# Performance work log

Measured on AMD Instinct MI355X. Metric: run time of the kernel, lower is better.

Reference implementation:

```python
import jax, jax.numpy as jnp
import numpy as np

N, E, IN, OUT, H = 100000, 1600000, 128, 128, 4
C = OUT // H
NEG_SLOPE = 0.2  # PyG GATConv default LeakyReLU slope
BN_EPS = 1e-5


def setup_inputs() -> dict:
    key = jax.random.key(0)
    k = jax.random.split(key, 6)
    x = jax.random.normal(k[0], (N, IN), dtype=jnp.float32)
    edge_index = jax.random.randint(k[1], (2, E), 0, N, dtype=jnp.int64)
    W = jax.random.normal(k[2], (IN, H * C), dtype=jnp.float32) / np.sqrt(IN)
    att_src = jax.random.normal(k[3], (H, C), dtype=jnp.float32) * 0.1
    att_dst = jax.random.normal(k[4], (H, C), dtype=jnp.float32) * 0.1
    gat_bias = jnp.zeros((H * C,), dtype=jnp.float32)
    bn_gamma = jnp.ones((OUT,), dtype=jnp.float32)
    bn_beta = jnp.zeros((OUT,), dtype=jnp.float32)
    return {"x": x, "edge_index": edge_index, "W": W, "att_src": att_src,
            "att_dst": att_dst, "gat_bias": gat_bias, "bn_gamma": bn_gamma,
            "bn_beta": bn_beta}


def reference(x, edge_index, W, att_src, att_dst, gat_bias, bn_gamma, bn_beta):
    n = x.shape[0]
    # GATConv: linear transform, per-head view [N,H,C]
    h = (x @ W).reshape(n, H, C)
    # add self loops (PyG default add_self_loops=True)
    loop = jnp.arange(n, dtype=edge_index.dtype)
    src = jnp.concatenate([edge_index[0], loop])  # message source j
    dst = jnp.concatenate([edge_index[1], loop])  # message target i
    # per-node attention logits [N,H]
    a_src = jnp.einsum('nhc,hc->nh', h, att_src)
    a_dst = jnp.einsum('nhc,hc->nh', h, att_dst)
    # per-edge logits [Etot,H], LeakyReLU, segment softmax over dst
    e = jax.nn.leaky_relu(a_src[src] + a_dst[dst], NEG_SLOPE)
    m = jax.ops.segment_max(e, dst, num_segments=n)
    e = jnp.exp(e - m[dst])
    s = jax.ops.segment_sum(e, dst, num_segments=n)
    alpha = e / (s[dst] + 1e-16)  # dropout(p=0.3) is identity at eval
    # weighted scatter-add aggregation
    msg = h[src] * alpha[:, :, None]  # [Etot,H,C]
    out = jax.ops.segment_sum(msg, dst, num_segments=n).reshape(n, H * C)
    out = out + gat_bias
    # BatchNorm1d (batch statistics, biased var)
    mean = jnp.mean(out, axis=0)
    var = jnp.var(out, axis=0)
    out = bn_gamma * (out - mean) * jax.lax.rsqrt(var + BN_EPS) + bn_beta
    # residual (proj is Identity since in_ch == out_ch) + ReLU
    return jax.nn.relu(out + x)
```

## Files before the change

### kernel.cpp

```cpp
#include <hip/hip_runtime.h>

#define NEG 0.2f
#define EPB 8192
#define NB64MAX 1568
#define CAPB_MAX 1536

typedef short short8 __attribute__((ext_vector_type(8)));
typedef float floatx4 __attribute__((ext_vector_type(4)));

__device__ __forceinline__ float bf_lo(unsigned int u) { return __uint_as_float(u << 16); }
__device__ __forceinline__ float bf_hi(unsigned int u) { return __uint_as_float(u & 0xffff0000u); }
__device__ __forceinline__ unsigned short f2bf(float f) {
    unsigned int u = __float_as_uint(f);
    return (unsigned short)((u + 0x7fff + ((u >> 16) & 1)) >> 16);
}

__global__ __launch_bounds__(256) void k_wconv(const float* __restrict__ W,
                                               unsigned short* __restrict__ Wtb) {
    int i = blockIdx.x * 256 + threadIdx.x;
    int n = i >> 7, k = i & 127;
    Wtb[n * 128 + k] = f2bf(W[k * 128 + n]);
}

__global__ __launch_bounds__(256) void k_gemm(const float* __restrict__ x,
                                              const unsigned short* __restrict__ Wtb,
                                              const float* __restrict__ att_src,
                                              const float* __restrict__ att_dst,
                                              unsigned short* __restrict__ hb,
                                              unsigned int* __restrict__ asd, int N) {
    __shared__ unsigned short As[64 * 128];
    __shared__ unsigned short Bs[128 * 128];
    int t = threadIdx.x;
    int r0 = blockIdx.x * 64;
#pragma unroll
    for (int p = 0; p < 8; p++) {
        int idx = t + 256 * p;
        int row = idx >> 5, c4 = idx & 31;
        float4 v = make_float4(0.f, 0.f, 0.f, 0.f);
        if (r0 + row < N) v = *(const float4*)&x[(size_t)(r0 + row) * 128 + c4 * 4];
        int kb = c4 >> 1;
        unsigned short* d = &As[row * 128 + ((kb ^ (row & 7)) << 3) + (c4 & 1) * 4];
        d[0] = f2bf(v.x); d[1] = f2bf(v.y); d[2] = f2bf(v.z); d[3] = f2bf(v.w);
    }
#pragma unroll
    for (int p = 0; p < 8; p++) {
        int idx = t + 256 * p;
        int n = idx >> 4, k8 = idx & 15;
        *(short8*)&Bs[n * 128 + ((k8 ^ (n & 7)) << 3)] = *(const short8*)&Wtb[n * 128 + k8 * 8];
    }
    __syncthreads();
    int lane = t & 63, wv = t >> 6;
    int m16 = lane & 15, quad = lane >> 4;
    int rowbase = wv * 16;
    floatx4 acc[8];
#pragma unroll
    for (int c = 0; c < 8; c++) acc[c] = (floatx4){0.f, 0.f, 0.f, 0.f};
#pragma unroll
    for (int ks = 0; ks < 4; ks++) {
        int arow = rowbase + m16;
        short8 a = *(const short8*)&As[arow * 128 + (((ks * 4 + quad) ^ (arow & 7)) << 3)];
#pragma unroll
        for (int c = 0; c < 8; c++) {
            int brow = c * 16 + m16;
            short8 b = *(const short8*)&Bs[brow * 128 + (((ks * 4 + quad) ^ (brow & 7)) << 3)];
            acc[c] = __builtin_amdgcn_mfma_f32_16x16x32_bf16(a, b, acc[c], 0, 0, 0);
        }
    }
    float ps[4][4], pd[4][4];
#pragma unroll
    for (int hd = 0; hd < 4; hd++)
#pragma unroll
        for (int r = 0; r < 4; r++) { ps[hd][r] = 0.f; pd[hd][r] = 0.f; }
#pragma unroll
    for (int c = 0; c < 8; c++) {
        int col = c * 16 + m16;
        float as_ = att_src[col], ad_ = att_dst[col];
        int hd = c >> 1;
#pragma unroll
        for (int r = 0; r < 4; r++) {
            float v = acc[c][r];
            int row = r0 + rowbase + quad * 4 + r;
            if (row < N) hb[(size_t)row * 128 + col] = f2bf(v);
            ps[hd][r] = fmaf(v, as_, ps[hd][r]);
            pd[hd][r] = fmaf(v, ad_, pd[hd][r]);
        }
    }
#pragma unroll
    for (int off = 1; off < 16; off <<= 1) {
#pragma unroll
        for (int hd = 0; hd < 4; hd++)
#pragma unroll
            for (int r = 0; r < 4; r++) {
                ps[hd][r] += __shfl_xor(ps[hd][r], off, 16);
                pd[hd][r] += __shfl_xor(pd[hd][r], off, 16);
            }
    }
    if (m16 == 0) {
#pragma unroll
        for (int r = 0; r < 4; r++) {
            int row = r0 + rowbase + quad * 4 + r;
            if (row < N)
#pragma unroll
                for (int hd = 0; hd < 4; hd++)
                    asd[row * 4 + hd] = ((unsigned int)f2bf(pd[hd][r]) << 16) | f2bf(ps[hd][r]);
        }
    }
}

__global__ __launch_bounds__(512) void k_bin3(const int* __restrict__ ei,
                                              int* __restrict__ gcur,
                                              unsigned int* __restrict__ pairs,
                                              int E, int NB, int CAPB) {
    __shared__ int cnt[NB64MAX];
    __shared__ int lbase[NB64MAX];
    int t = threadIdx.x;
    for (int i = t; i < NB; i += 512) cnt[i] = 0;
    __syncthreads();
    int base = blockIdx.x * EPB, end = min(base + EPB, E);
    for (int i = base + t; i < end; i += 512) atomicAdd(&cnt[ei[E + i] >> 6], 1);
    __syncthreads();
    for (int i = t; i < NB; i += 512) {
        int c = cnt[i];
        if (c) {
            int s = atomicAdd(&gcur[i], c);
            lbase[i] = (s + c <= CAPB) ? s : -1;
        }
    }
    __syncthreads();
    for (int i = base + t; i < end; i += 512) {
        int d = ei[E + i];
        int b = d >> 6;
        int lb = lbase[b];
        if (lb >= 0) {
            int slot = atomicSub(&cnt[b], 1) - 1;
            pairs[(size_t)b * CAPB + lb + slot] =
                (unsigned int)ei[i] | ((unsigned int)(d & 63) << 20);
        }
    }
}

__global__ __launch_bounds__(256) void k_agg2(const unsigned int* __restrict__ hb,
                                              const unsigned int* __restrict__ asd,
                                              const int* __restrict__ gcur,
                                              const unsigned int* __restrict__ pairs,
                                              unsigned int* __restrict__ yb,
                                              int N, int CAPB) {
    __shared__ unsigned int ent[CAPB_MAX];
    __shared__ int cnt64[64], off64[64], cur64[64], stmp[64];
    int b = blockIdx.x, t = threadIdx.x;
    size_t base = (size_t)b * CAPB;
    int cnt = min(gcur[b], CAPB);
    if (t < 64) cnt64[t] = 0;
    __syncthreads();
    for (int i = t; i < cnt; i += 256) atomicAdd(&cnt64[(pairs[base + i] >> 20) & 63], 1);
    __syncthreads();
    if (t < 64) stmp[t] = cnt64[t];
    __syncthreads();
    for (int d = 1; d < 64; d <<= 1) {
        int add = (t < 64 && t >= d) ? stmp[t - d] : 0;
        __syncthreads();
        if (t < 64) stmp[t] += add;
        __syncthreads();
    }
    if (t < 64) { int ex = stmp[t] - cnt64[t]; off64[t] = ex; cur64[t] = ex; }
    __syncthreads();
    for (int i = t; i < cnt; i += 256) {
        unsigned int e = pairs[base + i];
        int slot = atomicAdd(&cur64[(e >> 20) & 63], 1);
        ent[slot] = e & 0xFFFFFu;
    }
    __syncthreads();
    int lane = t & 63, wv = t >> 6;
    int head = lane >> 4, sub = lane & 15, wsel = lane & 48;
    for (int k = 0; k < 16; k++) {
        int ln = wv * 16 + k;
        int n = b * 64 + ln;
        if (n >= N) break;
        unsigned int au = asd[n * 4 + head];
        float adst = bf_hi(au);
        float e0 = bf_lo(au) + adst;
        e0 = e0 > 0.f ? e0 : NEG * e0;
        float w0 = __expf(e0);
        unsigned int hu = hb[(size_t)n * 64 + lane];
        float acc0 = w0 * bf_lo(hu), acc1 = w0 * bf_hi(hu), sw = w0;
        int st = off64[ln], c = cnt64[ln];
        int sjn = n;
        float evn = 0.f;
        if (sub < c) {
            sjn = (int)ent[st + sub];
            evn = bf_lo(asd[sjn * 4 + head]);
        }
        for (int eb = 0; eb < c; eb += 16) {
            int sj_l = sjn;
            float ev = evn + adst;
            ev = ev > 0.f ? ev : NEG * ev;
            float wl = (eb + sub < c) ? __expf(ev) : 0.f;
            if (eb + 16 + sub < c) {
                sjn = (int)ent[st + eb + 16 + sub];
                evn = bf_lo(asd[sjn * 4 + head]);
            } else sjn = n;
#pragma unroll
            for (int j = 0; j < 16; j++) {
                int sj = __shfl(sj_l, j, 64);
                float wj = __shfl(wl, wsel | j, 64);
                unsigned int hj = hb[(size_t)sj * 64 + lane];
                acc0 = fmaf(wj, bf_lo(hj), acc0);
                acc1 = fmaf(wj, bf_hi(hj), acc1);
                sw += wj;
            }
        }
        float inv = 1.0f / (sw + 1e-16f);
        yb[(size_t)n * 64 + lane] = ((unsigned int)f2bf(acc1 * inv) << 16) | f2bf(acc0 * inv);
    }
}

__global__ __launch_bounds__(256) void k_bnstats(const unsigned int* __restrict__ yb,
                                                 float* __restrict__ gsum,
                                                 float* __restrict__ gsumsq, int N) {
    __shared__ float s0[256], s1[256], s2[256], s3[256];
    int t = threadIdx.x;
    int cp = t & 63;
    int g = t >> 6;
    int r0 = blockIdx.x * 128 + g;
    float sl = 0.f, sh = 0.f, ql = 0.f, qh = 0.f;
#pragma unroll 4
    for (int i = 0; i < 32; i++) {
        int r = r0 + i * 4;
        if (r < N) {
            unsigned int u = yb[(size_t)r * 64 + cp];
            float lo = bf_lo(u), hi = bf_hi(u);
            sl += lo; sh += hi;
            ql = fmaf(lo, lo, ql);
            qh = fmaf(hi, hi, qh);
        }
    }
    s0[t] = sl; s1[t] = sh; s2[t] = ql; s3[t] = qh;
    __syncthreads();
    if (t < 64) {
        float a = s0[t] + s0[t + 64] + s0[t + 128] + s0[t + 192];
        float bb = s1[t] + s1[t + 64] + s1[t + 128] + s1[t + 192];
        float c = s2[t] + s2[t + 64] + s2[t + 128] + s2[t + 192];
        float d = s3[t] + s3[t + 64] + s3[t + 128] + s3[t + 192];
        atomicAdd(&gsum[2 * t], a);
        atomicAdd(&gsum[2 * t + 1], bb);
        atomicAdd(&gsumsq[2 * t], c);
        atomicAdd(&gsumsq[2 * t + 1], d);
    }
}

__global__ __launch_bounds__(128) void k_bnfinal(const float* __restrict__ gsum,
                                                 const float* __restrict__ gsumsq,
                                                 const float* __restrict__ gamma,
                                                 const float* __restrict__ beta,
                                                 float* __restrict__ scale,
                                                 float* __restrict__ shift, int N) {
    int c = threadIdx.x;
    if (c < 128) {
        float invN = 1.0f / (float)N;
        float mean = gsum[c] * invN;
        float var = gsumsq[c] * invN - mean * mean;
        float sc = gamma[c] * rsqrtf(var + 1e-5f);
        scale[c] = sc;
        shift[c] = beta[c] - mean * sc;
    }
}

__global__ __launch_bounds__(256) void k_final(const unsigned int* __restrict__ yb,
                                               const float* __restrict__ x,
                                               const float* __restrict__ scale,
                                               const float* __restrict__ shift,
                                               float* __restrict__ out, int total4) {
    int i = blockIdx.x * 256 + threadIdx.x;
    if (i >= total4) return;
    int c4 = i & 31;
    uint2 u = ((const uint2*)yb)[i];
    float4 xv = ((const float4*)x)[i];
    float4 sc = ((const float4*)scale)[c4];
    float4 sh = ((const float4*)shift)[c4];
    float4 r;
    r.x = fmaxf(fmaf(bf_lo(u.x), sc.x, sh.x) + xv.x, 0.f);
    r.y = fmaxf(fmaf(bf_hi(u.x), sc.y, sh.y) + xv.y, 0.f);
    r.z = fmaxf(fmaf(bf_lo(u.y), sc.z, sh.z) + xv.z, 0.f);
    r.w = fmaxf(fmaf(bf_hi(u.y), sc.w, sh.w) + xv.w, 0.f);
    ((float4*)out)[i] = r;
}

extern "C" void kernel_launch(void* const* d_in, const int* in_sizes, int n_in,
                              void* d_out, int out_size, void* d_ws, size_t ws_size,
                              hipStream_t stream) {
    const float* x       = (const float*)d_in[0];
    const int*   ei      = (const int*)d_in[1];
    const float* W       = (const float*)d_in[2];
    const float* att_src = (const float*)d_in[3];
    const float* att_dst = (const float*)d_in[4];
    const float* gamma   = (const float*)d_in[6];
    const float* beta    = (const float*)d_in[7];
    int N = in_sizes[0] / 128;
    int E = in_sizes[1] / 2;
    int NB = (N + 63) / 64;

    char* base = (char*)d_ws;
    size_t off = 0;
    auto alloc = [&](size_t b) -> char* {
        char* p = base + off;
        off = (off + b + 255) & ~(size_t)255;
        return p;
    };
    unsigned short* hb  = (unsigned short*)alloc((size_t)N * 128 * 2);
    unsigned int*   yb  = (unsigned int*)alloc((size_t)N * 64 * 4);
    unsigned int*   asd = (unsigned int*)alloc((size_t)N * 4 * 4);
    unsigned short* Wtb = (unsigned short*)alloc(128 * 128 * 2);
    int*   gcur   = (int*)alloc((size_t)NB * 4);
    float* gsum   = (float*)alloc(512);
    float* gsumsq = (float*)alloc(512);
    float* scale  = (float*)alloc(512);
    float* shift  = (float*)alloc(512);
    size_t rem = (ws_size > off) ? (ws_size - off) : 0;
    int CAPB = (int)((rem / ((size_t)NB * 4)) & ~(size_t)15);
    if (CAPB > CAPB_MAX) CAPB = CAPB_MAX;
    unsigned int* pairs = (unsigned int*)alloc((size_t)NB * CAPB * 4);
    float* outp = (float*)d_out;

    hipMemsetAsync(gcur, 0, (size_t)NB * 4, stream);
    hipMemsetAsync(gsum, 0, 512, stream);
    hipMemsetAsync(gsumsq, 0, 512, stream);

    int chunks = (E + EPB - 1) / EPB;
    k_wconv<<<64, 256, 0, stream>>>(W, Wtb);
    k_gemm<<<(N + 63) / 64, 256, 0, stream>>>(x, Wtb, att_src, att_dst, hb, asd, N);
    k_bin3<<<chunks, 512, 0, stream>>>(ei, gcur, pairs, E, NB, CAPB);
    k_agg2<<<NB, 256, 0, stream>>>((const unsigned int*)hb, asd, gcur, pairs, yb, N, CAPB);
    k_bnstats<<<(N + 127) / 128, 256, 0, stream>>>(yb, gsum, gsumsq, N);
    k_bnfinal<<<1, 128, 0, stream>>>(gsum, gsumsq, gamma, beta, scale, shift, N);
    k_final<<<(N * 32 + 255) / 256, 256, 0, stream>>>(yb, x, scale, shift, outp, N * 32);
}
```

Before: 325.6 us.

## Fuse BN statistics into aggregation, vectorize edge binning loads, stage neighbors in LDS

The BatchNorm sum and sum-of-squares reduction now happens inside the aggregation kernel, computed on the fp32 values before bf16 rounding. This drops a separate kernel launch and a full re-read of yb. The binning kernel loads its edge chunk once, as int4 vectors held in registers, instead of reading the destination array twice with scalar loads. In the aggregation loop, neighbor ids and weights are broadcast through a per-wave LDS buffer rather than shuffles, and the softmax denominator is reduced once per node instead of being accumulated per edge. Costs are higher register pressure and extra LDS traffic, and the BN statistics now come from unrounded values, which changes numerics slightly.

```diff
diff --git a/kernel.cpp b/kernel.cpp
--- a/kernel.cpp
+++ b/kernel.cpp
@@ -116,8 +116,26 @@
     int t = threadIdx.x;
     for (int i = t; i < NB; i += 512) cnt[i] = 0;
     __syncthreads();
-    int base = blockIdx.x * EPB, end = min(base + EPB, E);
-    for (int i = base + t; i < end; i += 512) atomicAdd(&cnt[ei[E + i] >> 6], 1);
+    int base = blockIdx.x * EPB;
+    const int* dp = ei + E;
+    int dv[16], sv[16];
+#pragma unroll
+    for (int p = 0; p < 4; p++) {
+        int e0 = base + p * 2048 + t * 4;
+        if (e0 + 3 < E) {
+            *(int4*)&dv[p * 4] = *(const int4*)&dp[e0];
+            *(int4*)&sv[p * 4] = *(const int4*)&ei[e0];
+        } else {
+#pragma unroll
+            for (int q = 0; q < 4; q++) {
+                dv[p * 4 + q] = (e0 + q < E) ? dp[e0 + q] : -1;
+                sv[p * 4 + q] = (e0 + q < E) ? ei[e0 + q] : 0;
+            }
+        }
+    }
+#pragma unroll
+    for (int i = 0; i < 16; i++)
+        if (dv[i] >= 0) atomicAdd(&cnt[dv[i] >> 6], 1);
     __syncthreads();
     for (int i = t; i < NB; i += 512) {
         int c = cnt[i];
@@ -127,26 +145,33 @@
         }
     }
     __syncthreads();
-    for (int i = base + t; i < end; i += 512) {
-        int d = ei[E + i];
-        int b = d >> 6;
-        int lb = lbase[b];
-        if (lb >= 0) {
-            int slot = atomicSub(&cnt[b], 1) - 1;
-            pairs[(size_t)b * CAPB + lb + slot] =
-                (unsigned int)ei[i] | ((unsigned int)(d & 63) << 20);
-        }
-    }
-}
-
-__global__ __launch_bounds__(256) void k_agg2(const unsigned int* __restrict__ hb,
+#pragma unroll
+    for (int i = 0; i < 16; i++) {
+        int d = dv[i];
+        if (d >= 0) {
+            int b = d >> 6;
+            int lb = lbase[b];
+            if (lb >= 0) {
+                int slot = atomicSub(&cnt[b], 1) - 1;
+                pairs[(size_t)b * CAPB + lb + slot] =
+                    (unsigned int)sv[i] | ((unsigned int)(d & 63) << 20);
+            }
+        }
+    }
+}
+
+__global__ __launch_bounds__(256) void k_agg3(const unsigned int* __restrict__ hb,
                                               const unsigned int* __restrict__ asd,
                                               const int* __restrict__ gcur,
                                               const unsigned int* __restrict__ pairs,
                                               unsigned int* __restrict__ yb,
+                                              float* __restrict__ gsum,
+                                              float* __restrict__ gsumsq,
                                               int N, int CAPB) {
     __shared__ unsigned int ent[CAPB_MAX];
     __shared__ int cnt64[64], off64[64], cur64[64], stmp[64];
+    __shared__ uint2 wsc[4][64];
+    __shared__ float2 bnS[4][64], bnQ[4][64];
     int b = blockIdx.x, t = threadIdx.x;
     size_t base = (size_t)b * CAPB;
     int cnt = min(gcur[b], CAPB);
@@ -171,80 +196,69 @@
     }
     __syncthreads();
     int lane = t & 63, wv = t >> 6;
-    int head = lane >> 4, sub = lane & 15, wsel = lane & 48;
+    int head = lane >> 4, sub = lane & 15;
+    float bns0 = 0.f, bns1 = 0.f, bnq0 = 0.f, bnq1 = 0.f;
     for (int k = 0; k < 16; k++) {
         int ln = wv * 16 + k;
         int n = b * 64 + ln;
-        if (n >= N) break;
-        unsigned int au = asd[n * 4 + head];
-        float adst = bf_hi(au);
-        float e0 = bf_lo(au) + adst;
-        e0 = e0 > 0.f ? e0 : NEG * e0;
-        float w0 = __expf(e0);
-        unsigned int hu = hb[(size_t)n * 64 + lane];
-        float acc0 = w0 * bf_lo(hu), acc1 = w0 * bf_hi(hu), sw = w0;
-        int st = off64[ln], c = cnt64[ln];
-        int sjn = n;
-        float evn = 0.f;
-        if (sub < c) {
-            sjn = (int)ent[st + sub];
-            evn = bf_lo(asd[sjn * 4 + head]);
-        }
-        for (int eb = 0; eb < c; eb += 16) {
-            int sj_l = sjn;
-            float ev = evn + adst;
-            ev = ev > 0.f ? ev : NEG * ev;
-            float wl = (eb + sub < c) ? __expf(ev) : 0.f;
-            if (eb + 16 + sub < c) {
-                sjn = (int)ent[st + eb + 16 + sub];
-                evn = bf_lo(asd[sjn * 4 + head]);
-            } else sjn = n;
-#pragma unroll
-            for (int j = 0; j < 16; j++) {
-                int sj = __shfl(sj_l, j, 64);
-                float wj = __shfl(wl, wsel | j, 64);
-                unsigned int hj = hb[(size_t)sj * 64 + lane];
-                acc0 = fmaf(wj, bf_lo(hj), acc0);
-                acc1 = fmaf(wj, bf_hi(hj), acc1);
-                sw += wj;
-            }
-        }
-        float inv = 1.0f / (sw + 1e-16f);
-        yb[(size_t)n * 64 + lane] = ((unsigned int)f2bf(acc1 * inv) << 16) | f2bf(acc0 * inv);
-    }
-}
-
-__global__ __launch_bounds__(256) void k_bnstats(const unsigned int* __restrict__ yb,
-                                                 float* __restrict__ gsum,
-                                                 float* __restrict__ gsumsq, int N) {
-    __shared__ float s0[256], s1[256], s2[256], s3[256];
-    int t = threadIdx.x;
-    int cp = t & 63;
-    int g = t >> 6;
-    int r0 = blockIdx.x * 128 + g;
-    float sl = 0.f, sh = 0.f, ql = 0.f, qh = 0.f;
-#pragma unroll 4
-    for (int i = 0; i < 32; i++) {
-        int r = r0 + i * 4;
-        if (r < N) {
-            unsigned int u = yb[(size_t)r * 64 + cp];
-            float lo = bf_lo(u), hi = bf_hi(u);
-            sl += lo; sh += hi;
-            ql = fmaf(lo, lo, ql);
-            qh = fmaf(hi, hi, qh);
-        }
-    }
-    s0[t] = sl; s1[t] = sh; s2[t] = ql; s3[t] = qh;
+        if (n < N) {
+            unsigned int au = asd[(n << 2) + head];
+            float adst = bf_hi(au);
+            float e0 = bf_lo(au) + adst;
+            e0 = e0 > 0.f ? e0 : NEG * e0;
+            float w0 = __expf(e0);
+            unsigned int hu = hb[(n << 6) + lane];
+            float acc0 = w0 * bf_lo(hu), acc1 = w0 * bf_hi(hu);
+            float swp = 0.f;
+            int st = off64[ln], c = cnt64[ln];
+            int sjc = n;
+            float rawc = 0.f;
+            if (sub < c) {
+                sjc = (int)ent[st + sub];
+                rawc = bf_lo(asd[(sjc << 2) + head]);
+            }
+            for (int eb = 0; eb < c; eb += 16) {
+                float ev = rawc + adst;
+                ev = ev > 0.f ? ev : NEG * ev;
+                float wc = (eb + sub < c) ? __expf(ev) : 0.f;
+                swp += wc;
+                wsc[wv][lane] = make_uint2((unsigned int)sjc, __float_as_uint(wc));
+                __builtin_amdgcn_wave_barrier();
+                if (eb + 16 + sub < c) {
+                    sjc = (int)ent[st + eb + 16 + sub];
+                    rawc = bf_lo(asd[(sjc << 2) + head]);
+                } else { sjc = n; rawc = 0.f; }
+#pragma unroll
+                for (int j = 0; j < 16; j++) {
+                    uint2 p = wsc[wv][(lane & 48) | j];
+                    unsigned int hj = hb[(p.x << 6) + lane];
+                    float wj = __uint_as_float(p.y);
+                    acc0 = fmaf(wj, bf_lo(hj), acc0);
+                    acc1 = fmaf(wj, bf_hi(hj), acc1);
+                }
+                __builtin_amdgcn_wave_barrier();
+            }
+#pragma unroll
+            for (int off2 = 8; off2; off2 >>= 1) swp += __shfl_xor(swp, off2, 16);
+            float sw = swp + w0;
+            float inv = 1.0f / (sw + 1e-16f);
+            float v0 = acc0 * inv, v1 = acc1 * inv;
+            yb[(n << 6) + lane] = ((unsigned int)f2bf(v1) << 16) | f2bf(v0);
+            bns0 += v0; bns1 += v1;
+            bnq0 = fmaf(v0, v0, bnq0);
+            bnq1 = fmaf(v1, v1, bnq1);
+        }
+    }
+    bnS[wv][lane] = make_float2(bns0, bns1);
+    bnQ[wv][lane] = make_float2(bnq0, bnq1);
     __syncthreads();
     if (t < 64) {
-        float a = s0[t] + s0[t + 64] + s0[t + 128] + s0[t + 192];
-        float bb = s1[t] + s1[t + 64] + s1[t + 128] + s1[t + 192];
-        float c = s2[t] + s2[t + 64] + s2[t + 128] + s2[t + 192];
-        float d = s3[t] + s3[t + 64] + s3[t + 128] + s3[t + 192];
-        atomicAdd(&gsum[2 * t], a);
-        atomicAdd(&gsum[2 * t + 1], bb);
-        atomicAdd(&gsumsq[2 * t], c);
-        atomicAdd(&gsumsq[2 * t + 1], d);
+        float2 s0 = bnS[0][t], s1 = bnS[1][t], s2 = bnS[2][t], s3 = bnS[3][t];
+        float2 q0 = bnQ[0][t], q1 = bnQ[1][t], q2 = bnQ[2][t], q3 = bnQ[3][t];
+        atomicAdd(&gsum[2 * t],     s0.x + s1.x + s2.x + s3.x);
+        atomicAdd(&gsum[2 * t + 1], s0.y + s1.y + s2.y + s3.y);
+        atomicAdd(&gsumsq[2 * t],     q0.x + q1.x + q2.x + q3.x);
+        atomicAdd(&gsumsq[2 * t + 1], q0.y + q1.y + q2.y + q3.y);
     }
 }
 
@@ -311,10 +325,10 @@
     unsigned int*   asd = (unsigned int*)alloc((size_t)N * 4 * 4);
     unsigned short* Wtb = (unsigned short*)alloc(128 * 128 * 2);
     int*   gcur   = (int*)alloc((size_t)NB * 4);
-    float* gsum   = (float*)alloc(512);
-    float* gsumsq = (float*)alloc(512);
+    float* bnbuf  = (float*)alloc(256 * 4);
     float* scale  = (float*)alloc(512);
     float* shift  = (float*)alloc(512);
+    float* gsum = bnbuf, *gsumsq = bnbuf + 128;
     size_t rem = (ws_size > off) ? (ws_size - off) : 0;
     int CAPB = (int)((rem / ((size_t)NB * 4)) & ~(size_t)15);
     if (CAPB > CAPB_MAX) CAPB = CAPB_MAX;
@@ -322,15 +336,14 @@
     float* outp = (float*)d_out;
 
     hipMemsetAsync(gcur, 0, (size_t)NB * 4, stream);
-    hipMemsetAsync(gsum, 0, 512, stream);
-    hipMemsetAsync(gsumsq, 0, 512, stream);
+    hipMemsetAsync(bnbuf, 0, 256 * 4, stream);
 
     int chunks = (E + EPB - 1) / EPB;
     k_wconv<<<64, 256, 0, stream>>>(W, Wtb);
     k_gemm<<<(N + 63) / 64, 256, 0, stream>>>(x, Wtb, att_src, att_dst, hb, asd, N);
     k_bin3<<<chunks, 512, 0, stream>>>(ei, gcur, pairs, E, NB, CAPB);
-    k_agg2<<<NB, 256, 0, stream>>>((const unsigned int*)hb, asd, gcur, pairs, yb, N, CAPB);
-    k_bnstats<<<(N + 127) / 128, 256, 0, stream>>>(yb, gsum, gsumsq, N);
+    k_agg3<<<NB, 256, 0, stream>>>((const unsigned int*)hb, asd, gcur, pairs, yb,
+                                   gsum, gsumsq, N, CAPB);
     k_bnfinal<<<1, 128, 0, stream>>>(gsum, gsumsq, gamma, beta, scale, shift, N);
     k_final<<<(N * 32 + 255) / 256, 256, 0, stream>>>(yb, x, scale, shift, outp, N * 32);
 }
```

Result: slower. 334.5 us (+2.8%).
